# Optimization experiments

Hardware: AMD Instinct MI355X
Metric: run time of the kernel (lower is better)

The kernel has to match this reference:

```python
import jax, jax.numpy as jnp
import numpy as np

B, L, F, P, E, H, D, C, V = 256, 100, 8, 4, 64, 4, 64, 32, 10000
HD = H * D  # 256 = att_dim * head_num
TOWER_IN = F * E + F * E + P * E + C  # 1312
LN_EPS = 1e-3  # keras LayerNormalization default epsilon


def _ln(x, g, b):
    m = jnp.mean(x, axis=-1, keepdims=True)
    v = jnp.mean(jnp.square(x - m), axis=-1, keepdims=True)
    return (x - m) * jax.lax.rsqrt(v + LN_EPS) * g + b


def setup_inputs() -> dict:
    key = jax.random.key(0)
    ks = jax.random.split(key, 32)
    w = lambda k, s: jax.random.normal(k, s, jnp.float32) * 0.02
    inp = {
        'target_ad': jax.random.randint(ks[0], (B, F), 0, V),
        'ubs_feature': jax.random.randint(ks[1], (B, L, F), 0, V),
        'profile_feature': jax.random.randint(ks[2], (B, P), 0, V),
        'context_feature': jax.random.normal(ks[3], (B, C), jnp.float32),
        # embedding tables: one per sparse feature, stacked
        'item_tables': w(ks[4], (F, V, E)),
        'profile_tables': w(ks[5], (P, V, E)),
        # per-timestep distinct attention weights, stacked over L
        'q_w': w(ks[6], (L, E, HD)),
        'k_w': w(ks[7], (L, E, HD)),
        'v_w': w(ks[8], (L, E, HD)),
        'lin_w': w(ks[9], (L, HD, E)),
        'lin_b': jnp.zeros((L, E), jnp.float32),
        # shared post-attention layernorm
        'ln_g': jnp.ones((E,), jnp.float32),
        'ln_b': jnp.zeros((E,), jnp.float32),
        # dense tower
        't_w1': w(ks[10], (TOWER_IN, 1024)), 't_b1': jnp.zeros((1024,), jnp.float32),
        't_g1': jnp.ones((1024,), jnp.float32), 't_bb1': jnp.zeros((1024,), jnp.float32),
        't_w2': w(ks[11], (1024, 512)), 't_b2': jnp.zeros((512,), jnp.float32),
        't_g2': jnp.ones((512,), jnp.float32), 't_bb2': jnp.zeros((512,), jnp.float32),
        't_w3': w(ks[12], (512, 256)), 't_b3': jnp.zeros((256,), jnp.float32),
        't_g3': jnp.ones((256,), jnp.float32), 't_bb3': jnp.zeros((256,), jnp.float32),
        't_w4': w(ks[13], (256, 1)), 't_b4': jnp.zeros((1,), jnp.float32),
    }
    return inp


def reference(target_ad, ubs_feature, profile_feature, context_feature,
              item_tables, profile_tables, q_w, k_w, v_w, lin_w, lin_b,
              ln_g, ln_b,
              t_w1, t_b1, t_g1, t_bb1,
              t_w2, t_b2, t_g2, t_bb2,
              t_w3, t_b3, t_g3, t_bb3,
              t_w4, t_b4):
    b = target_ad.shape[0]
    # embedding lookups (feature-wise tables)
    te = item_tables[jnp.arange(F)[None, :], target_ad]              # [B,F,E]
    ue = item_tables[jnp.arange(F)[None, None, :], ubs_feature]      # [B,L,F,E]
    pe = profile_tables[jnp.arange(P)[None, :], profile_feature]     # [B,P,E]

    # per-step distinct Q/K/V projections, batched over L via einsum
    q = jnp.einsum('blfe,leo->blfo', ue, q_w).reshape(b, L, F, H, D)
    k = jnp.einsum('blfe,leo->blfo', ue, k_w).reshape(b, L, F, H, D)
    v = jnp.einsum('blfe,leo->blfo', ue, v_w).reshape(b, L, F, H, D)
    scores = jnp.einsum('blfhd,blghd->blhfg', q, k) / jnp.sqrt(jnp.float32(D))
    attw = jax.nn.softmax(scores, axis=-1)                           # [B,L,H,F,F]
    att = jnp.einsum('blhfg,blghd->blfhd', attw, v).reshape(b, L, F, HD)
    att_out = jnp.einsum('blfo,loe->blfe', att, lin_w) + lin_b[None, :, None, :]
    # shared LayerNorm per step, summed over L (original accumulates into zeros_like)
    ubs_t = jnp.sum(_ln(att_out, ln_g, ln_b), axis=1)                # [B,F,E]
    ubs = jax.nn.relu(ubs_t / jnp.float32(L))

    total = jnp.concatenate([ubs.reshape(b, -1), te.reshape(b, -1),
                             pe.reshape(b, -1), context_feature], axis=-1)

    h = jax.nn.relu(_ln(total @ t_w1 + t_b1, t_g1, t_bb1))
    h = jax.nn.relu(_ln(h @ t_w2 + t_b2, t_g2, t_bb2))
    h = jax.nn.relu(_ln(h @ t_w3 + t_b3, t_g3, t_bb3))
    out = jax.nn.sigmoid(h @ t_w4 + t_b4)                            # [B,1]
    return out
```

## Files before the change

kernel.cpp:

```cpp
#include <hip/hip_runtime.h>
#include <hip/hip_bf16.h>

#define B_ 256
#define L_ 100
#define F_ 8
#define P_ 4
#define E_ 64
#define H_ 4
#define D_ 64
#define C_ 32
#define V_ 10000
#define TOWER_IN_ 1312
#define LN_EPS 0.001f
#define LCH_ 4
#define NCH_ 25
#define ZK_ 40

typedef __attribute__((ext_vector_type(8))) short bf8v;
typedef __attribute__((ext_vector_type(8))) unsigned short us8;
typedef __attribute__((ext_vector_type(4))) float f4v;

__device__ __forceinline__ unsigned short f2bf(float x) {
    __hip_bfloat16 h = __float2bfloat16(x);
    return __builtin_bit_cast(unsigned short, h);
}

#define BARRIER() do { \
    asm volatile("s_waitcnt lgkmcnt(0)" ::: "memory"); \
    __builtin_amdgcn_s_barrier(); \
    asm volatile("" ::: "memory"); \
} while (0)

__global__ __launch_bounds__(256) void precomp_kernel(
    const float* __restrict__ q_w, const float* __restrict__ k_w,
    const float* __restrict__ v_w, const float* __restrict__ lin_w,
    unsigned short* __restrict__ wsMT, unsigned short* __restrict__ wsWT)
{
    __shared__ float sA[64][65];
    __shared__ float sB[64][65];
    const int t = threadIdx.x;
    const int l = blockIdx.x >> 2;
    const int h = blockIdx.x & 3;
    const size_t obase = (size_t)(l * 4 + h) * 4096;

    for (int i = 0; i < 16; ++i) {
        int idx = t + i * 256;
        int e = idx >> 6, d = idx & 63;
        sA[e][d] = q_w[(l * 64 + e) * 256 + h * 64 + d];
        sB[e][d] = k_w[(l * 64 + e) * 256 + h * 64 + d];
    }
    __syncthreads();
    for (int i = 0; i < 16; ++i) {
        int idx = t + i * 256;
        int o = idx >> 6, e = idx & 63;
        float s = 0.f;
        #pragma unroll 8
        for (int d = 0; d < 64; ++d) s += sA[e][d] * sB[o][d];
        wsMT[obase + idx] = f2bf(s);
    }
    __syncthreads();

    for (int i = 0; i < 16; ++i) {
        int idx = t + i * 256;
        int dd = idx >> 6, oo = idx & 63;
        sB[dd][oo] = lin_w[l * 16384 + (h * 64 + dd) * 64 + oo];
    }
    for (int i = 0; i < 16; ++i) {
        int idx = t + i * 256;
        int e = idx >> 6, d = idx & 63;
        sA[e][d] = v_w[(l * 64 + e) * 256 + h * 64 + d];
    }
    __syncthreads();
    for (int i = 0; i < 16; ++i) {
        int idx = t + i * 256;
        int o = idx >> 6, e = idx & 63;
        float s = 0.f;
        #pragma unroll 8
        for (int d = 0; d < 64; ++d) s += sA[e][d] * sB[d][o];
        wsWT[obase + idx] = f2bf(s);
    }
}

__global__ __launch_bounds__(256) void prep_kernel(
    const float* __restrict__ w1, const float* __restrict__ w2,
    const float* __restrict__ w3,
    unsigned short* __restrict__ Wt1, unsigned short* __restrict__ Wt2,
    unsigned short* __restrict__ Wt3)
{
    __shared__ float tile[32][33];
    int bx = blockIdx.x;
    const float* src; unsigned short* dst; int K, N, tk, tn;
    if (bx < 1312)      { src = w1; dst = Wt1; K = 1312; N = 1024; tk = bx / 32;  tn = bx % 32; }
    else if (bx < 1824) { int i = bx - 1312; src = w2; dst = Wt2; K = 1024; N = 512; tk = i / 16; tn = i % 16; }
    else                { int i = bx - 1824; src = w3; dst = Wt3; K = 512;  N = 256; tk = i / 8;  tn = i % 8; }
    const int k0 = tk * 32, n0 = tn * 32;
    const int rr = threadIdx.x >> 5, cc = threadIdx.x & 31;
    #pragma unroll
    for (int i = 0; i < 4; ++i) {
        int r = rr * 4 + i;
        tile[r][cc] = src[(size_t)(k0 + r) * N + n0 + cc];
    }
    __syncthreads();
    #pragma unroll
    for (int i = 0; i < 4; ++i) {
        int r = rr * 4 + i;
        dst[(size_t)(n0 + r) * K + k0 + cc] = f2bf(tile[cc][r]);
    }
}

__global__ __launch_bounds__(256, 3) void attn_kernel(
    const int* __restrict__ ubs_feature, const float* __restrict__ item_tables,
    const unsigned short* __restrict__ wsMT, const unsigned short* __restrict__ wsWT,
    const float* __restrict__ lin_b, const float* __restrict__ ln_g,
    const float* __restrict__ ln_b, float* __restrict__ ubs_acc)
{
    __shared__ __align__(16) unsigned short sUE[64][72];
    __shared__ __align__(16) unsigned short sT[64][136];
    __shared__ __align__(16) unsigned short sZt[4][64][ZK_];
    __shared__ __align__(16) unsigned short sAblk[4][16][32];
    __shared__ float sLng[64], sLnb[64], sLinb[LCH_][64];

    const int t = threadIdx.x;
    const int c = blockIdx.x >> 5;
    const int b0 = (blockIdx.x & 31) * 8;
    const int wv = t >> 6, lane = t & 63, quad = lane >> 4, cl = lane & 15;
    const int role = wv >> 1, hlw = wv & 1;

    const int grow = wv * 16 + (lane >> 2);
    const int gseg = lane & 3;
    const int gb = b0 + (grow >> 3), gf = grow & 7;

    if (t < 64) { sLng[t] = ln_g[t]; sLnb[t] = ln_b[t]; }
    if (t >= 64 && t < 128) {
        #pragma unroll
        for (int li = 0; li < LCH_; ++li)
            sLinb[li][t - 64] = lin_b[(c * LCH_ + li) * 64 + (t - 64)];
    }

    int vidx[LCH_];
    #pragma unroll
    for (int li = 0; li < LCH_; ++li)
        vidx[li] = ubs_feature[(gb * L_ + c * LCH_ + li) * F_ + gf];

    float4 pf[4];
    bf8v bfrag[4][2];

    auto load_bfrag = [&](int lh) {
        const unsigned short* Bsrc = (role == 0 ? wsMT : wsWT) + ((size_t)lh * 4096);
        #pragma unroll
        for (int nt = 0; nt < 4; ++nt)
            #pragma unroll
            for (int k2 = 0; k2 < 2; ++k2)
                bfrag[nt][k2] = *(const bf8v*)(Bsrc + (nt * 16 + cl) * 64 + k2 * 32 + quad * 8);
    };
    auto load_pf = [&](int li) {
        const float* srcp = item_tables + ((size_t)gf * V_ + vidx[li]) * 64 + gseg * 16;
        #pragma unroll
        for (int j = 0; j < 4; ++j) pf[j] = ((const float4*)srcp)[j];
    };
    auto store_ue = [&]() {
        us8 u0, u1;
        u0[0] = f2bf(pf[0].x); u0[1] = f2bf(pf[0].y); u0[2] = f2bf(pf[0].z); u0[3] = f2bf(pf[0].w);
        u0[4] = f2bf(pf[1].x); u0[5] = f2bf(pf[1].y); u0[6] = f2bf(pf[1].z); u0[7] = f2bf(pf[1].w);
        u1[0] = f2bf(pf[2].x); u1[1] = f2bf(pf[2].y); u1[2] = f2bf(pf[2].z); u1[3] = f2bf(pf[2].w);
        u1[4] = f2bf(pf[3].x); u1[5] = f2bf(pf[3].y); u1[6] = f2bf(pf[3].z); u1[7] = f2bf(pf[3].w);
        *(us8*)&sUE[grow][gseg * 16]     = u0;
        *(us8*)&sUE[grow][gseg * 16 + 8] = u1;
    };

    load_pf(0);
    load_bfrag((c * LCH_) * 4 + hlw);
    store_ue();
    BARRIER();

    float lnacc[16];
    #pragma unroll
    for (int i = 0; i < 16; ++i) lnacc[i] = 0.f;

    for (int li = 0; li < LCH_; ++li) {
        const int l = c * LCH_ + li;

        if (li + 1 < LCH_) load_pf(li + 1);

        f4v accO[4];
        #pragma unroll
        for (int nt = 0; nt < 4; ++nt) accO[nt] = {0.f, 0.f, 0.f, 0.f};

        #pragma unroll
        for (int half = 0; half < 2; ++half) {
            #pragma unroll
            for (int m = 0; m < 4; ++m) {
                bf8v a0 = *(const bf8v*)&sUE[m * 16 + cl][quad * 8];
                bf8v a1 = *(const bf8v*)&sUE[m * 16 + cl][32 + quad * 8];
                #pragma unroll
                for (int nt = 0; nt < 4; ++nt) {
                    f4v acc = {0.f, 0.f, 0.f, 0.f};
                    acc = __builtin_amdgcn_mfma_f32_16x16x32_bf16(a0, bfrag[nt][0], acc, 0, 0, 0);
                    acc = __builtin_amdgcn_mfma_f32_16x16x32_bf16(a1, bfrag[nt][1], acc, 0, 0, 0);
                    if (role == 0) {
                        #pragma unroll
                        for (int j = 0; j < 4; ++j)
                            sT[m * 16 + quad * 4 + j][hlw * 64 + nt * 16 + cl] = f2bf(acc[j]);
                    } else {
                        ushort4 zp;
                        zp.x = f2bf(acc[0]); zp.y = f2bf(acc[1]);
                        zp.z = f2bf(acc[2]); zp.w = f2bf(acc[3]);
                        const int k0 = (quad >> 1) * 16 + hlw * 8 + (quad & 1) * 4;
                        *(ushort4*)&sZt[m][nt * 16 + cl][k0] = zp;
                    }
                }
            }
            if (half == 0)            load_bfrag(l * 4 + 2 + hlw);
            else if (li + 1 < LCH_)   load_bfrag((l + 1) * 4 + hlw);
            BARRIER();

            {
                const int p = wv;
                const bool valid = (cl >> 3) == (quad >> 1);
                #pragma unroll
                for (int hl = 0; hl < 2; ++hl) {
                    bf8v a0s = *(const bf8v*)&sT[p * 16 + cl][hl * 64 + quad * 8];
                    bf8v a1s = *(const bf8v*)&sT[p * 16 + cl][hl * 64 + 32 + quad * 8];
                    bf8v u0 = *(const bf8v*)&sUE[p * 16 + cl][quad * 8];
                    bf8v u1 = *(const bf8v*)&sUE[p * 16 + cl][32 + quad * 8];
                    f4v acc = {0.f, 0.f, 0.f, 0.f};
                    acc = __builtin_amdgcn_mfma_f32_16x16x32_bf16(a0s, u0, acc, 0, 0, 0);
                    acc = __builtin_amdgcn_mfma_f32_16x16x32_bf16(a1s, u1, acc, 0, 0, 0);
                    const int kk = hl * 8 + (cl & 7) + (cl >> 3) * 16;
                    #pragma unroll
                    for (int j = 0; j < 4; ++j) {
                        float v = acc[j] * 0.125f;
                        float mx = v;
                        mx = fmaxf(mx, __shfl_xor(mx, 1));
                        mx = fmaxf(mx, __shfl_xor(mx, 2));
                        mx = fmaxf(mx, __shfl_xor(mx, 4));
                        float ex = __expf(v - mx);
                        float sm = ex;
                        sm += __shfl_xor(sm, 1);
                        sm += __shfl_xor(sm, 2);
                        sm += __shfl_xor(sm, 4);
                        float aw = valid ? ex * __builtin_amdgcn_rcpf(sm) : 0.f;
                        sAblk[p][quad * 4 + j][kk] = f2bf(aw);
                    }
                }
            }

            {
                const int p = wv;
                bf8v a0p = *(const bf8v*)&sAblk[p][cl][quad * 8];
                #pragma unroll
                for (int nt = 0; nt < 4; ++nt) {
                    bf8v bz = *(const bf8v*)&sZt[p][nt * 16 + cl][quad * 8];
                    accO[nt] = __builtin_amdgcn_mfma_f32_16x16x32_bf16(a0p, bz, accO[nt], 0, 0, 0);
                }
            }
            BARRIER();
        }

        {
            float x[16];
            #pragma unroll
            for (int nt = 0; nt < 4; ++nt)
                #pragma unroll
                for (int j = 0; j < 4; ++j)
                    x[nt * 4 + j] = accO[nt][j] + sLinb[li][nt * 16 + cl];
            #pragma unroll
            for (int j = 0; j < 4; ++j) {
                float s = x[j] + x[4 + j] + x[8 + j] + x[12 + j];
                #pragma unroll
                for (int m = 1; m < 16; m <<= 1) s += __shfl_xor(s, m);
                float mean = s * (1.f / 64.f);
                float q = 0.f;
                #pragma unroll
                for (int nt = 0; nt < 4; ++nt) { float d = x[nt * 4 + j] - mean; q += d * d; }
                #pragma unroll
                for (int m = 1; m < 16; m <<= 1) q += __shfl_xor(q, m);
                float rst = rsqrtf(q * (1.f / 64.f) + LN_EPS);
                #pragma unroll
                for (int nt = 0; nt < 4; ++nt) {
                    int col = nt * 16 + cl;
                    lnacc[nt * 4 + j] += (x[nt * 4 + j] - mean) * rst * sLng[col] + sLnb[col];
                }
            }
        }

        if (li + 1 < LCH_) {
            store_ue();
            BARRIER();
        }
    }

    #pragma unroll
    for (int j = 0; j < 4; ++j) {
        const int row = wv * 16 + quad * 4 + j;
        const int b = b0 + (row >> 3), f = row & 7;
        #pragma unroll
        for (int nt = 0; nt < 4; ++nt)
            atomicAdd(&ubs_acc[(size_t)b * 512 + f * 64 + nt * 16 + cl], lnacc[nt * 4 + j]);
    }
}

__device__ __forceinline__ float block_reduce_sum(float v, float* sRed) {
    #pragma unroll
    for (int m = 1; m < 64; m <<= 1) v += __shfl_xor(v, m, 64);
    int wave = threadIdx.x >> 6, lane = threadIdx.x & 63;
    __syncthreads();
    if (lane == 0) sRed[wave] = v;
    __syncthreads();
    return sRed[0] + sRed[1] + sRed[2] + sRed[3];
}

__global__ __launch_bounds__(256) void reduceX_kernel(
    const float* __restrict__ ubs_acc,
    const int* __restrict__ target_ad, const int* __restrict__ profile_feature,
    const float* __restrict__ context,
    const float* __restrict__ item_tables, const float* __restrict__ profile_tables,
    unsigned short* __restrict__ X)
{
    const int b = blockIdx.x, t = threadIdx.x;
    const float2 v = *(const float2*)(ubs_acc + (size_t)b * 512 + t * 2);
    X[b * TOWER_IN_ + t * 2]     = f2bf(fmaxf(v.x * 0.01f, 0.f));
    X[b * TOWER_IN_ + t * 2 + 1] = f2bf(fmaxf(v.y * 0.01f, 0.f));
    for (int cc = 512 + t; cc < TOWER_IN_; cc += 256) {
        float x;
        if (cc < 1024) { int j = cc - 512, f = j >> 6, e = j & 63;
            x = item_tables[((size_t)f * V_ + target_ad[b * 8 + f]) * 64 + e]; }
        else if (cc < 1280) { int j = cc - 1024, pp = j >> 6, e = j & 63;
            x = profile_tables[((size_t)pp * V_ + profile_feature[b * 4 + pp]) * 64 + e]; }
        else x = context[b * 32 + (cc - 1280)];
        X[b * TOWER_IN_ + cc] = f2bf(x);
    }
}

__global__ __launch_bounds__(256) void gemm_kernel(
    const unsigned short* __restrict__ A, const unsigned short* __restrict__ Bw,
    const float* __restrict__ bias, float* __restrict__ C, int K, int N)
{
    const int t = threadIdx.x;
    const int wv = t >> 6, lane = t & 63, quad = lane >> 4, cl = lane & 15;
    const int n0 = blockIdx.x * 64 + wv * 16;
    const int m0 = blockIdx.y * 16;
    f4v acc0 = {0.f, 0.f, 0.f, 0.f};
    f4v acc1 = {0.f, 0.f, 0.f, 0.f};
    const unsigned short* arow = A + (size_t)(m0 + cl) * K + quad * 8;
    const unsigned short* brow = Bw + (size_t)(n0 + cl) * K + quad * 8;
    int k0 = 0;
    #pragma unroll 2
    for (; k0 + 64 <= K; k0 += 64) {
        bf8v a0 = *(const bf8v*)(arow + k0);
        bf8v b0 = *(const bf8v*)(brow + k0);
        bf8v a1 = *(const bf8v*)(arow + k0 + 32);
        bf8v b1 = *(const bf8v*)(brow + k0 + 32);
        acc0 = __builtin_amdgcn_mfma_f32_16x16x32_bf16(a0, b0, acc0, 0, 0, 0);
        acc1 = __builtin_amdgcn_mfma_f32_16x16x32_bf16(a1, b1, acc1, 0, 0, 0);
    }
    if (k0 < K) {
        bf8v a = *(const bf8v*)(arow + k0);
        bf8v b = *(const bf8v*)(brow + k0);
        acc0 = __builtin_amdgcn_mfma_f32_16x16x32_bf16(a, b, acc0, 0, 0, 0);
    }
    float bv = bias[n0 + cl];
    #pragma unroll
    for (int j = 0; j < 4; ++j)
        C[(size_t)(m0 + quad * 4 + j) * N + n0 + cl] = acc0[j] + acc1[j] + bv;
}

__global__ __launch_bounds__(256) void ln_relu_kernel(
    const float* __restrict__ C, const float* __restrict__ g,
    const float* __restrict__ bb, unsigned short* __restrict__ Hx, int N)
{
    __shared__ float sRed[4];
    const int b = blockIdx.x, t = threadIdx.x;
    float s = 0.f, s2 = 0.f;
    for (int j = t; j < N; j += 256) { float x = C[(size_t)b * N + j]; s += x; s2 += x * x; }
    s  = block_reduce_sum(s,  sRed);
    __syncthreads();
    s2 = block_reduce_sum(s2, sRed);
    float invN = 1.f / (float)N;
    float mean = s * invN;
    float var  = s2 * invN - mean * mean;
    float rst  = rsqrtf(fmaxf(var, 0.f) + LN_EPS);
    for (int j = t; j < N; j += 256) {
        float x = C[(size_t)b * N + j];
        Hx[(size_t)b * N + j] = f2bf(fmaxf((x - mean) * rst * g[j] + bb[j], 0.f));
    }
}

__global__ __launch_bounds__(256) void final_kernel(
    const float* __restrict__ C3, const float* __restrict__ g3,
    const float* __restrict__ bb3, const float* __restrict__ w4,
    const float* __restrict__ b4, float* __restrict__ out)
{
    __shared__ float sRed[4];
    const int b = blockIdx.x, t = threadIdx.x;
    float x = C3[b * 256 + t];
    float s = block_reduce_sum(x, sRed);
    float mean = s * (1.f / 256.f);
    float d = x - mean;
    __syncthreads();
    float q = block_reduce_sum(d * d, sRed);
    float rst = rsqrtf(q * (1.f / 256.f) + LN_EPS);
    float h = fmaxf(d * rst * g3[t] + bb3[t], 0.f);
    __syncthreads();
    float p = block_reduce_sum(h * w4[t], sRed);
    if (t == 0) out[b] = 1.f / (1.f + expf(-(p + b4[0])));
}

extern "C" void kernel_launch(void* const* d_in, const int* in_sizes, int n_in,
                              void* d_out, int out_size, void* d_ws, size_t ws_size,
                              hipStream_t stream)
{
    (void)in_sizes; (void)n_in; (void)out_size; (void)ws_size;
    const int*   target_ad       = (const int*)d_in[0];
    const int*   ubs_feature     = (const int*)d_in[1];
    const int*   profile_feature = (const int*)d_in[2];
    const float* context         = (const float*)d_in[3];
    const float* item_tables     = (const float*)d_in[4];
    const float* profile_tables  = (const float*)d_in[5];
    const float* q_w   = (const float*)d_in[6];
    const float* k_w   = (const float*)d_in[7];
    const float* v_w   = (const float*)d_in[8];
    const float* lin_w = (const float*)d_in[9];
    const float* lin_b = (const float*)d_in[10];
    const float* ln_g  = (const float*)d_in[11];
    const float* ln_b  = (const float*)d_in[12];
    const float* t_w1  = (const float*)d_in[13];
    const float* t_b1  = (const float*)d_in[14];
    const float* t_g1  = (const float*)d_in[15];
    const float* t_bb1 = (const float*)d_in[16];
    const float* t_w2  = (const float*)d_in[17];
    const float* t_b2  = (const float*)d_in[18];
    const float* t_g2  = (const float*)d_in[19];
    const float* t_bb2 = (const float*)d_in[20];
    const float* t_w3  = (const float*)d_in[21];
    const float* t_b3  = (const float*)d_in[22];
    const float* t_g3  = (const float*)d_in[23];
    const float* t_bb3 = (const float*)d_in[24];
    const float* t_w4  = (const float*)d_in[25];
    const float* t_b4  = (const float*)d_in[26];

    char* ws = (char*)d_ws;
    unsigned short* wsMT = (unsigned short*)(ws);
    unsigned short* wsWT = (unsigned short*)(ws +  3276800);
    float* ubs_acc       = (float*)         (ws +  6553600);
    unsigned short* Wt1  = (unsigned short*)(ws +  7077888);
    unsigned short* Wt2  = (unsigned short*)(ws +  9764864);
    unsigned short* Wt3  = (unsigned short*)(ws + 10813440);
    unsigned short* X    = (unsigned short*)(ws + 11075584);
    float*          C1   = (float*)         (ws + 11747328);
    unsigned short* H1   = (unsigned short*)(ws + 12795904);
    float*          C2   = (float*)         (ws + 13320192);
    unsigned short* H2   = (unsigned short*)(ws + 13844480);
    float*          C3   = (float*)         (ws + 14106624);

    hipMemsetAsync(ubs_acc, 0, B_ * F_ * E_ * sizeof(float), stream);

    prep_kernel<<<1952, 256, 0, stream>>>(t_w1, t_w2, t_w3, Wt1, Wt2, Wt3);
    precomp_kernel<<<L_ * H_, 256, 0, stream>>>(q_w, k_w, v_w, lin_w, wsMT, wsWT);
    attn_kernel<<<NCH_ * 32, 256, 0, stream>>>(ubs_feature, item_tables, wsMT, wsWT,
                                               lin_b, ln_g, ln_b, ubs_acc);
    reduceX_kernel<<<B_, 256, 0, stream>>>(ubs_acc, target_ad, profile_feature, context,
                                           item_tables, profile_tables, X);
    gemm_kernel<<<dim3(16, 16), 256, 0, stream>>>(X,  Wt1, t_b1, C1, 1312, 1024);
    ln_relu_kernel<<<B_, 256, 0, stream>>>(C1, t_g1, t_bb1, H1, 1024);
    gemm_kernel<<<dim3(8, 16),  256, 0, stream>>>(H1, Wt2, t_b2, C2, 1024, 512);
    ln_relu_kernel<<<B_, 256, 0, stream>>>(C2, t_g2, t_bb2, H2, 512);
    gemm_kernel<<<dim3(4, 16),  256, 0, stream>>>(H2, Wt3, t_b3, C3, 512, 256);
    final_kernel<<<B_, 256, 0, stream>>>(C3, t_g3, t_bb3, t_w4, t_b4, (float*)d_out);
}
```

Measured before the change: 274.8 us.

## Merge weight-prep kernels, register-tile precompute, fold LayerNorm stats into GEMM epilogue

```diff
diff --git a/kernel.cpp b/kernel.cpp
--- a/kernel.cpp
+++ b/kernel.cpp
@@ -31,80 +31,123 @@
     asm volatile("" ::: "memory"); \
 } while (0)
 
-__global__ __launch_bounds__(256) void precomp_kernel(
+__global__ __launch_bounds__(256) void prologue_kernel(
     const float* __restrict__ q_w, const float* __restrict__ k_w,
     const float* __restrict__ v_w, const float* __restrict__ lin_w,
-    unsigned short* __restrict__ wsMT, unsigned short* __restrict__ wsWT)
-{
-    __shared__ float sA[64][65];
-    __shared__ float sB[64][65];
-    const int t = threadIdx.x;
-    const int l = blockIdx.x >> 2;
-    const int h = blockIdx.x & 3;
-    const size_t obase = (size_t)(l * 4 + h) * 4096;
-
-    for (int i = 0; i < 16; ++i) {
-        int idx = t + i * 256;
-        int e = idx >> 6, d = idx & 63;
-        sA[e][d] = q_w[(l * 64 + e) * 256 + h * 64 + d];
-        sB[e][d] = k_w[(l * 64 + e) * 256 + h * 64 + d];
-    }
-    __syncthreads();
-    for (int i = 0; i < 16; ++i) {
-        int idx = t + i * 256;
-        int o = idx >> 6, e = idx & 63;
-        float s = 0.f;
-        #pragma unroll 8
-        for (int d = 0; d < 64; ++d) s += sA[e][d] * sB[o][d];
-        wsMT[obase + idx] = f2bf(s);
-    }
-    __syncthreads();
-
-    for (int i = 0; i < 16; ++i) {
-        int idx = t + i * 256;
-        int dd = idx >> 6, oo = idx & 63;
-        sB[dd][oo] = lin_w[l * 16384 + (h * 64 + dd) * 64 + oo];
-    }
-    for (int i = 0; i < 16; ++i) {
-        int idx = t + i * 256;
-        int e = idx >> 6, d = idx & 63;
-        sA[e][d] = v_w[(l * 64 + e) * 256 + h * 64 + d];
-    }
-    __syncthreads();
-    for (int i = 0; i < 16; ++i) {
-        int idx = t + i * 256;
-        int o = idx >> 6, e = idx & 63;
-        float s = 0.f;
-        #pragma unroll 8
-        for (int d = 0; d < 64; ++d) s += sA[e][d] * sB[d][o];
-        wsWT[obase + idx] = f2bf(s);
-    }
-}
-
-__global__ __launch_bounds__(256) void prep_kernel(
+    unsigned short* __restrict__ wsMT, unsigned short* __restrict__ wsWT,
     const float* __restrict__ w1, const float* __restrict__ w2,
     const float* __restrict__ w3,
     unsigned short* __restrict__ Wt1, unsigned short* __restrict__ Wt2,
-    unsigned short* __restrict__ Wt3)
-{
-    __shared__ float tile[32][33];
-    int bx = blockIdx.x;
-    const float* src; unsigned short* dst; int K, N, tk, tn;
-    if (bx < 1312)      { src = w1; dst = Wt1; K = 1312; N = 1024; tk = bx / 32;  tn = bx % 32; }
-    else if (bx < 1824) { int i = bx - 1312; src = w2; dst = Wt2; K = 1024; N = 512; tk = i / 16; tn = i % 16; }
-    else                { int i = bx - 1824; src = w3; dst = Wt3; K = 512;  N = 256; tk = i / 8;  tn = i % 8; }
-    const int k0 = tk * 32, n0 = tn * 32;
-    const int rr = threadIdx.x >> 5, cc = threadIdx.x & 31;
-    #pragma unroll
-    for (int i = 0; i < 4; ++i) {
-        int r = rr * 4 + i;
-        tile[r][cc] = src[(size_t)(k0 + r) * N + n0 + cc];
-    }
-    __syncthreads();
-    #pragma unroll
-    for (int i = 0; i < 4; ++i) {
-        int r = rr * 4 + i;
-        dst[(size_t)(n0 + r) * K + k0 + cc] = f2bf(tile[cc][r]);
+    unsigned short* __restrict__ Wt3, float* __restrict__ ubs_acc)
+{
+    __shared__ float sA[64][68];
+    __shared__ float sB[64][68];
+    const int t = threadIdx.x;
+    const int bx = blockIdx.x;
+
+    if (bx < 400) {
+        const int l = bx >> 2;
+        const int h = bx & 3;
+        const size_t obase = (size_t)(l * 4 + h) * 4096;
+        const int te = t & 15, to = t >> 4;
+
+        for (int i = 0; i < 16; ++i) {
+            int idx = t + i * 256;
+            int e = idx >> 6, d = idx & 63;
+            sA[e][d] = q_w[(l * 64 + e) * 256 + h * 64 + d];
+            sB[e][d] = k_w[(l * 64 + e) * 256 + h * 64 + d];
+        }
+        __syncthreads();
+        {
+            float acc[4][4];
+            #pragma unroll
+            for (int i = 0; i < 4; ++i)
+                #pragma unroll
+                for (int j = 0; j < 4; ++j) acc[i][j] = 0.f;
+            for (int d0 = 0; d0 < 64; d0 += 4) {
+                float4 a4[4], b4[4];
+                #pragma unroll
+                for (int i = 0; i < 4; ++i) a4[i] = *(const float4*)&sA[te + 16 * i][d0];
+                #pragma unroll
+                for (int j = 0; j < 4; ++j) b4[j] = *(const float4*)&sB[to + 16 * j][d0];
+                #pragma unroll
+                for (int i = 0; i < 4; ++i)
+                    #pragma unroll
+                    for (int j = 0; j < 4; ++j) {
+                        acc[i][j] += a4[i].x * b4[j].x;
+                        acc[i][j] += a4[i].y * b4[j].y;
+                        acc[i][j] += a4[i].z * b4[j].z;
+                        acc[i][j] += a4[i].w * b4[j].w;
+                    }
+            }
+            #pragma unroll
+            for (int j = 0; j < 4; ++j)
+                #pragma unroll
+                for (int i = 0; i < 4; ++i)
+                    wsMT[obase + (to + 16 * j) * 64 + (te + 16 * i)] = f2bf(acc[i][j]);
+        }
+        __syncthreads();
+
+        for (int i = 0; i < 16; ++i) {
+            int idx = t + i * 256;
+            int e = idx >> 6, d = idx & 63;
+            sA[e][d] = v_w[(l * 64 + e) * 256 + h * 64 + d];
+            int oo = idx & 63, dd = idx >> 6;
+            sB[oo][dd] = lin_w[l * 16384 + (h * 64 + dd) * 64 + oo];
+        }
+        __syncthreads();
+        {
+            float acc[4][4];
+            #pragma unroll
+            for (int i = 0; i < 4; ++i)
+                #pragma unroll
+                for (int j = 0; j < 4; ++j) acc[i][j] = 0.f;
+            for (int d0 = 0; d0 < 64; d0 += 4) {
+                float4 a4[4], b4[4];
+                #pragma unroll
+                for (int i = 0; i < 4; ++i) a4[i] = *(const float4*)&sA[te + 16 * i][d0];
+                #pragma unroll
+                for (int j = 0; j < 4; ++j) b4[j] = *(const float4*)&sB[to + 16 * j][d0];
+                #pragma unroll
+                for (int i = 0; i < 4; ++i)
+                    #pragma unroll
+                    for (int j = 0; j < 4; ++j) {
+                        acc[i][j] += a4[i].x * b4[j].x;
+                        acc[i][j] += a4[i].y * b4[j].y;
+                        acc[i][j] += a4[i].z * b4[j].z;
+                        acc[i][j] += a4[i].w * b4[j].w;
+                    }
+            }
+            #pragma unroll
+            for (int j = 0; j < 4; ++j)
+                #pragma unroll
+                for (int i = 0; i < 4; ++i)
+                    wsWT[obase + (to + 16 * j) * 64 + (te + 16 * i)] = f2bf(acc[i][j]);
+        }
+    } else if (bx < 2352) {
+        float (*tile)[33] = (float (*)[33])sA;
+        int bi = bx - 400;
+        const float* src; unsigned short* dst; int K, N, tk, tn;
+        if (bi < 1312)      { src = w1; dst = Wt1; K = 1312; N = 1024; tk = bi / 32;  tn = bi % 32; }
+        else if (bi < 1824) { int i = bi - 1312; src = w2; dst = Wt2; K = 1024; N = 512; tk = i / 16; tn = i % 16; }
+        else                { int i = bi - 1824; src = w3; dst = Wt3; K = 512;  N = 256; tk = i / 8;  tn = i % 8; }
+        const int k0 = tk * 32, n0 = tn * 32;
+        const int rr = t >> 5, cc = t & 31;
+        #pragma unroll
+        for (int i = 0; i < 4; ++i) {
+            int r = rr * 4 + i;
+            tile[r][cc] = src[(size_t)(k0 + r) * N + n0 + cc];
+        }
+        __syncthreads();
+        #pragma unroll
+        for (int i = 0; i < 4; ++i) {
+            int r = rr * 4 + i;
+            dst[(size_t)(n0 + r) * K + k0 + cc] = f2bf(tile[cc][r]);
+        }
+    } else {
+        const int bi = bx - 2352;
+        float4 z = {0.f, 0.f, 0.f, 0.f};
+        *(float4*)(ubs_acc + (size_t)bi * 1024 + t * 4) = z;
     }
 }
 
@@ -300,24 +343,19 @@
     }
 }
 
-__device__ __forceinline__ float block_reduce_sum(float v, float* sRed) {
-    #pragma unroll
-    for (int m = 1; m < 64; m <<= 1) v += __shfl_xor(v, m, 64);
-    int wave = threadIdx.x >> 6, lane = threadIdx.x & 63;
-    __syncthreads();
-    if (lane == 0) sRed[wave] = v;
-    __syncthreads();
-    return sRed[0] + sRed[1] + sRed[2] + sRed[3];
-}
-
 __global__ __launch_bounds__(256) void reduceX_kernel(
     const float* __restrict__ ubs_acc,
     const int* __restrict__ target_ad, const int* __restrict__ profile_feature,
     const float* __restrict__ context,
     const float* __restrict__ item_tables, const float* __restrict__ profile_tables,
-    unsigned short* __restrict__ X)
+    unsigned short* __restrict__ X, float* __restrict__ statsAll)
 {
     const int b = blockIdx.x, t = threadIdx.x;
+    if (b == B_) {
+        float4 z = {0.f, 0.f, 0.f, 0.f};
+        ((float4*)statsAll)[t] = z;
+        return;
+    }
     const float2 v = *(const float2*)(ubs_acc + (size_t)b * 512 + t * 2);
     X[b * TOWER_IN_ + t * 2]     = f2bf(fmaxf(v.x * 0.01f, 0.f));
     X[b * TOWER_IN_ + t * 2 + 1] = f2bf(fmaxf(v.y * 0.01f, 0.f));
@@ -334,7 +372,8 @@
 
 __global__ __launch_bounds__(256) void gemm_kernel(
     const unsigned short* __restrict__ A, const unsigned short* __restrict__ Bw,
-    const float* __restrict__ bias, float* __restrict__ C, int K, int N)
+    const float* __restrict__ bias, float* __restrict__ C, int K, int N,
+    float* __restrict__ stats)
 {
     const int t = threadIdx.x;
     const int wv = t >> 6, lane = t & 63, quad = lane >> 4, cl = lane & 15;
@@ -360,30 +399,56 @@
         acc0 = __builtin_amdgcn_mfma_f32_16x16x32_bf16(a, b, acc0, 0, 0, 0);
     }
     float bv = bias[n0 + cl];
+    float cj[4];
     #pragma unroll
-    for (int j = 0; j < 4; ++j)
-        C[(size_t)(m0 + quad * 4 + j) * N + n0 + cl] = acc0[j] + acc1[j] + bv;
-}
-
-__global__ __launch_bounds__(256) void ln_relu_kernel(
-    const float* __restrict__ C, const float* __restrict__ g,
-    const float* __restrict__ bb, unsigned short* __restrict__ Hx, int N)
-{
-    __shared__ float sRed[4];
+    for (int j = 0; j < 4; ++j) {
+        cj[j] = acc0[j] + acc1[j] + bv;
+        C[(size_t)(m0 + quad * 4 + j) * N + n0 + cl] = cj[j];
+    }
+    if (stats) {
+        #pragma unroll
+        for (int j = 0; j < 4; ++j) {
+            float s = cj[j], q = cj[j] * cj[j];
+            #pragma unroll
+            for (int m = 1; m < 16; m <<= 1) { s += __shfl_xor(s, m); q += __shfl_xor(q, m); }
+            if (cl == 0) {
+                const int row = m0 + quad * 4 + j;
+                atomicAdd(&stats[row * 2], s);
+                atomicAdd(&stats[row * 2 + 1], q);
+            }
+        }
+    }
+}
+
+__global__ __launch_bounds__(256) void lnapply_kernel(
+    const float* __restrict__ C, const float* __restrict__ stats,
+    const float* __restrict__ g, const float* __restrict__ bb,
+    unsigned short* __restrict__ Hx, int N, float invN)
+{
     const int b = blockIdx.x, t = threadIdx.x;
-    float s = 0.f, s2 = 0.f;
-    for (int j = t; j < N; j += 256) { float x = C[(size_t)b * N + j]; s += x; s2 += x * x; }
-    s  = block_reduce_sum(s,  sRed);
+    const float s = stats[b * 2], q = stats[b * 2 + 1];
+    const float mean = s * invN;
+    const float var  = q * invN - mean * mean;
+    const float rst  = rsqrtf(fmaxf(var, 0.f) + LN_EPS);
+    for (int j = t * 4; j < N; j += 1024) {
+        float4 x = *(const float4*)(C + (size_t)b * N + j);
+        ushort4 o;
+        o.x = f2bf(fmaxf((x.x - mean) * rst * g[j]     + bb[j],     0.f));
+        o.y = f2bf(fmaxf((x.y - mean) * rst * g[j + 1] + bb[j + 1], 0.f));
+        o.z = f2bf(fmaxf((x.z - mean) * rst * g[j + 2] + bb[j + 2], 0.f));
+        o.w = f2bf(fmaxf((x.w - mean) * rst * g[j + 3] + bb[j + 3], 0.f));
+        *(ushort4*)(Hx + (size_t)b * N + j) = o;
+    }
+}
+
+__device__ __forceinline__ float block_reduce_sum(float v, float* sRed) {
+    #pragma unroll
+    for (int m = 1; m < 64; m <<= 1) v += __shfl_xor(v, m, 64);
+    int wave = threadIdx.x >> 6, lane = threadIdx.x & 63;
     __syncthreads();
-    s2 = block_reduce_sum(s2, sRed);
-    float invN = 1.f / (float)N;
-    float mean = s * invN;
-    float var  = s2 * invN - mean * mean;
-    float rst  = rsqrtf(fmaxf(var, 0.f) + LN_EPS);
-    for (int j = t; j < N; j += 256) {
-        float x = C[(size_t)b * N + j];
-        Hx[(size_t)b * N + j] = f2bf(fmaxf((x - mean) * rst * g[j] + bb[j], 0.f));
-    }
+    if (lane == 0) sRed[wave] = v;
+    __syncthreads();
+    return sRed[0] + sRed[1] + sRed[2] + sRed[3];
 }
 
 __global__ __launch_bounds__(256) void final_kernel(
@@ -452,19 +517,19 @@
     float*          C2   = (float*)         (ws + 13320192);
     unsigned short* H2   = (unsigned short*)(ws + 13844480);
     float*          C3   = (float*)         (ws + 14106624);
-
-    hipMemsetAsync(ubs_acc, 0, B_ * F_ * E_ * sizeof(float), stream);
-
-    prep_kernel<<<1952, 256, 0, stream>>>(t_w1, t_w2, t_w3, Wt1, Wt2, Wt3);
-    precomp_kernel<<<L_ * H_, 256, 0, stream>>>(q_w, k_w, v_w, lin_w, wsMT, wsWT);
+    float* stats1        = (float*)(ws);
+    float* stats2        = (float*)(ws + 2048);
+
+    prologue_kernel<<<2480, 256, 0, stream>>>(q_w, k_w, v_w, lin_w, wsMT, wsWT,
+                                              t_w1, t_w2, t_w3, Wt1, Wt2, Wt3, ubs_acc);
     attn_kernel<<<NCH_ * 32, 256, 0, stream>>>(ubs_feature, item_tables, wsMT, wsWT,
                                                lin_b, ln_g, ln_b, ubs_acc);
-    reduceX_kernel<<<B_, 256, 0, stream>>>(ubs_acc, target_ad, profile_feature, context,
-                                           item_tables, profile_tables, X);
-    gemm_kernel<<<dim3(16, 16), 256, 0, stream>>>(X,  Wt1, t_b1, C1, 1312, 1024);
-    ln_relu_kernel<<<B_, 256, 0, stream>>>(C1, t_g1, t_bb1, H1, 1024);
-    gemm_kernel<<<dim3(8, 16),  256, 0, stream>>>(H1, Wt2, t_b2, C2, 1024, 512);
-    ln_relu_kernel<<<B_, 256, 0, stream>>>(C2, t_g2, t_bb2, H2, 512);
-    gemm_kernel<<<dim3(4, 16),  256, 0, stream>>>(H2, Wt3, t_b3, C3, 512, 256);
+    reduceX_kernel<<<B_ + 1, 256, 0, stream>>>(ubs_acc, target_ad, profile_feature, context,
+                                               item_tables, profile_tables, X, stats1);
+    gemm_kernel<<<dim3(16, 16), 256, 0, stream>>>(X,  Wt1, t_b1, C1, 1312, 1024, stats1);
+    lnapply_kernel<<<B_, 256, 0, stream>>>(C1, stats1, t_g1, t_bb1, H1, 1024, 1.f / 1024.f);
+    gemm_kernel<<<dim3(8, 16),  256, 0, stream>>>(H1, Wt2, t_b2, C2, 1024, 512, stats2);
+    lnapply_kernel<<<B_, 256, 0, stream>>>(C2, stats2, t_g2, t_bb2, H2, 512, 1.f / 512.f);
+    gemm_kernel<<<dim3(4, 16),  256, 0, stream>>>(H2, Wt3, t_b3, C3, 512, 256, (float*)nullptr);
     final_kernel<<<B_, 256, 0, stream>>>(C3, t_g3, t_bb3, t_w4, t_b4, (float*)d_out);
 }
```

Result: faster. 265.6 us (-3.4%).
